# Kernel tuning notes

Measured on AMD Instinct MI355X. Metric: run time of the kernel, lower is better.

## Reference

```python
import jax, jax.numpy as jnp
import numpy as np
import math

N_NODES = 50000
N_EDGES = 1600000
C = 256
H = 8
HD = C // H


def setup_inputs() -> dict:
    key = jax.random.key(0)
    ks = jax.random.split(key, 16)
    s = 0.02
    d = {
        "feat": jax.random.normal(ks[0], (N_NODES, C), jnp.float32),
        "edge_src": jax.random.randint(ks[1], (N_EDGES,), 0, N_NODES),
        "edge_dst": jax.random.randint(ks[2], (N_EDGES,), 0, N_NODES),
        # torch nn.Linear weights are [out, in]
        "Wq": jax.random.normal(ks[3], (C, C), jnp.float32) * s,
        "bq": jnp.zeros((C,), jnp.float32),
        "Wk": jax.random.normal(ks[4], (C, C), jnp.float32) * s,
        "bk": jnp.zeros((C,), jnp.float32),
        "Wv": jax.random.normal(ks[5], (C, C), jnp.float32) * s,
        "bv": jnp.zeros((C,), jnp.float32),
        "Wp": jax.random.normal(ks[6], (C, C), jnp.float32) * s,
        "bp": jnp.zeros((C,), jnp.float32),
        "ln_g": jnp.ones((C,), jnp.float32),
        "ln_b": jnp.zeros((C,), jnp.float32),
        "W1": jax.random.normal(ks[7], (4 * C, C), jnp.float32) * s,
        "b1": jnp.zeros((4 * C,), jnp.float32),
        "W2": jax.random.normal(ks[8], (C, 4 * C), jnp.float32) * s,
        "b2": jnp.zeros((C,), jnp.float32),
    }
    return d


def _layernorm(x, g, b, eps=1e-5):
    mu = jnp.mean(x, axis=-1, keepdims=True)
    var = jnp.mean(jnp.square(x - mu), axis=-1, keepdims=True)
    return (x - mu) * jax.lax.rsqrt(var + eps) * g + b


def reference(feat, edge_src, edge_dst, Wq, bq, Wk, bk, Wv, bv, Wp, bp,
              ln_g, ln_b, W1, b1, W2, b2):
    n = feat.shape[0]
    q = (feat @ Wq.T + bq).reshape(n, H, HD)
    k = (feat @ Wk.T + bk).reshape(n, H, HD)
    v = (feat @ Wv.T + bv).reshape(n, H, HD)

    # per-edge attention logits: (q[dst] * k[src]).sum(-1) / sqrt(head_dim), clamped
    score = jnp.einsum('ehd,ehd->eh', q[edge_dst], k[edge_src])  # [E, H]
    score = jnp.clip(score / math.sqrt(HD), -10.0, 10.0)

    # destination-grouped (segment) softmax over incoming edges
    smax = jax.ops.segment_max(score, edge_dst, num_segments=n)
    smax = jnp.where(jnp.isfinite(smax), smax, 0.0)  # guard empty segments
    ex = jnp.exp(score - smax[edge_dst])
    den = jax.ops.segment_sum(ex, edge_dst, num_segments=n)
    alpha = ex / den[edge_dst]  # [E, H]

    # weighted scatter-aggregate: sum_e alpha_e * v[src_e] into dst
    wv = jax.ops.segment_sum(alpha[:, :, None] * v[edge_src], edge_dst,
                             num_segments=n).reshape(n, C)

    y = wv @ Wp.T + bp
    x = feat + y
    h = _layernorm(x, ln_g, ln_b)
    h = jax.nn.gelu(h @ W1.T + b1, approximate=False) @ W2.T + b2
    return x + h
```

## Files before the change

### kernel.cpp

```cpp
#include <hip/hip_runtime.h>
#include <hip/hip_bf16.h>

#define CDIM 256
#define NH 8
#define HDIM 32

typedef short bf8 __attribute__((ext_vector_type(8)));
typedef float f32x4 __attribute__((ext_vector_type(4)));
typedef float f32x2 __attribute__((ext_vector_type(2)));

__device__ __forceinline__ float bf2f(ushort u) {
  union { unsigned int i; float f; } x; x.i = ((unsigned int)u) << 16; return x.f;
}
__device__ __forceinline__ ushort f2bf(float f) {
  union { float f; unsigned int i; } x; x.f = f;
  unsigned int lsb = (x.i >> 16) & 1u;
  unsigned int r = x.i + 0x7fffu + lsb;
  return (ushort)(r >> 16);
}

__device__ __forceinline__ float dec_e4m3_sw(unsigned int b) {
  unsigned int s = b >> 7, e = (b >> 3) & 15, m = b & 7;
  float v = (e == 0) ? (float)m * 0.001953125f
                     : (float)(8 + m) * 0.125f * exp2f((float)((int)e - 7));
  return s ? -v : v;
}
__device__ __forceinline__ unsigned char enc_e4m3_sw(float f) {
  union { float f; unsigned int u; } x; x.f = f;
  unsigned int s = (x.u >> 31) << 7;
  float a = fabsf(f);
  if (!(a > 0.f)) return (unsigned char)s;
  if (a > 448.f) a = 448.f;
  int e = 0; float mant = frexpf(a, &e);
  int E = e + 6;
  unsigned int out;
  if (E <= 0) {
    int m = (int)rintf(a * 512.f);
    out = (m > 7) ? (s | (1u << 3)) : (s | (unsigned)m);
  } else {
    int m = (int)rintf(mant * 16.f);
    if (m == 16) { m = 8; E++; }
    if (E > 15 || (E == 15 && m - 8 > 6)) { E = 15; m = 14; }
    out = s | ((unsigned)E << 3) | (unsigned)(m - 8);
  }
  return (unsigned char)out;
}
template <bool HI>
__device__ __forceinline__ f32x2 fp8x2_f32(unsigned int w) {
#if __has_builtin(__builtin_amdgcn_cvt_pk_f32_fp8)
  return __builtin_amdgcn_cvt_pk_f32_fp8(w, HI);
#else
  unsigned int b0 = HI ? ((w >> 16) & 0xffu) : (w & 0xffu);
  unsigned int b1 = HI ? (w >> 24) : ((w >> 8) & 0xffu);
  f32x2 r; r[0] = dec_e4m3_sw(b0); r[1] = dec_e4m3_sw(b1); return r;
#endif
}
__device__ __forceinline__ unsigned char f32_fp8(float f) {
#if __has_builtin(__builtin_amdgcn_cvt_pk_fp8_f32)
  return (unsigned char)(__builtin_amdgcn_cvt_pk_fp8_f32(f, f, 0, false) & 0xff);
#else
  return enc_e4m3_sw(f);
#endif
}

__device__ __forceinline__ float fast_gelu(float t) {
  float u = 0.7978845608028654f * (t + 0.044715f * t * t * t);
  float ez = __expf(2.f * u);
  float th = 1.f - 2.f * __builtin_amdgcn_rcpf(ez + 1.f);
  return 0.5f * t * (1.f + th);
}

__device__ __forceinline__ void gload_lds16(const ushort* g, ushort* l) {
  __builtin_amdgcn_global_load_lds((const __attribute__((address_space(1))) unsigned int*)g,
                                   (__attribute__((address_space(3))) unsigned int*)l,
                                   16, 0, 0);
}

__global__ void k_cast4(const float4* __restrict__ s, ushort4* __restrict__ d, int n4) {
  int i = blockIdx.x * blockDim.x + threadIdx.x;
  if (i < n4) {
    float4 v = s[i];
    ushort4 o;
    o.x = f2bf(v.x); o.y = f2bf(v.y); o.z = f2bf(v.z); o.w = f2bf(v.w);
    d[i] = o;
  }
}

__global__ void k_hist(const int* __restrict__ dst, int E, int* __restrict__ deg) {
  int i = blockIdx.x * blockDim.x + threadIdx.x;
  if (i < E) atomicAdd(&deg[dst[i]], 1);
}

__global__ __launch_bounds__(1024) void k_scan1(const int* __restrict__ deg, int N,
                                                int* __restrict__ rowptr, int* __restrict__ bsum) {
  __shared__ int s[1024];
  int t = threadIdx.x;
  int i = blockIdx.x * 1024 + t;
  int val = (i < N) ? deg[i] : 0;
  s[t] = val;
  __syncthreads();
  for (int off = 1; off < 1024; off <<= 1) {
    int add = (t >= off) ? s[t - off] : 0;
    __syncthreads();
    s[t] += add;
    __syncthreads();
  }
  if (i < N) rowptr[i + 1] = s[t];
  if (t == 1023) bsum[blockIdx.x] = s[t];
}

__global__ void k_scan2(int* __restrict__ bsum, int nb) {
  if (threadIdx.x == 0 && blockIdx.x == 0) {
    int run = 0;
    for (int j = 0; j < nb; ++j) { int t = bsum[j]; bsum[j] = run; run += t; }
  }
}

__global__ void k_scan3(int* __restrict__ rowptr, const int* __restrict__ bsum, int N) {
  int i = blockIdx.x * blockDim.x + threadIdx.x;
  if (i < N) rowptr[i + 1] += bsum[i >> 10];
  if (i == 0) rowptr[0] = 0;
}

__global__ void k_scatter(const int* __restrict__ src, const int* __restrict__ dst, int E,
                          const int* __restrict__ rowptr, int* __restrict__ cur,
                          int* __restrict__ csr_src) {
  int i = blockIdx.x * blockDim.x + threadIdx.x;
  if (i < E) {
    int d = dst[i];
    int pos = rowptr[d] + atomicAdd(&cur[d], 1);
    csr_src[pos] = src[i];
  }
}

__device__ __forceinline__ void stageA8(const ushort* __restrict__ S, int ld,
                                        int r0, int nr, int k0,
                                        ushort* lds, int wave, int lane) {
  int g = wave * 64 + lane;
  int row = g >> 2, slot = g & 3;
  int rr = r0 + row; rr = (rr < nr) ? rr : (nr - 1);
  const ushort* src = S + (size_t)rr * ld + k0 + ((slot ^ (row & 3)) << 3);
  gload_lds16(src, &lds[(size_t)(wave * 64) * 8]);
}

__device__ __forceinline__ void stageB8(const ushort* __restrict__ S, int ld,
                                        int r0, int nr, int k0,
                                        ushort* lds, int wave, int lane) {
#pragma unroll
  for (int j = 0; j < 2; ++j) {
    int g = wave * 128 + j * 64 + lane;
    int row = g >> 2, slot = g & 3;
    int rr = r0 + row; rr = (rr < nr) ? rr : (nr - 1);
    const ushort* src = S + (size_t)rr * ld + k0 + ((slot ^ (row & 3)) << 3);
    gload_lds16(src, &lds[(size_t)(wave * 128 + j * 64) * 8]);
  }
}

__device__ __forceinline__ void gemm256_core(const ushort* __restrict__ A, int lda, int rowt, int nA,
                                             const ushort* __restrict__ B, int ldb, int colt, int nB,
                                             int K, ushort* lA, ushort* lB, f32x4* acc) {
  int tid = threadIdx.x;
  int wave = tid >> 6, lane = tid & 63;
  int m = lane & 15, quad = lane >> 4;
  int r0w = (wave & 1) * 64, c0w = (wave >> 1) * 64;
  int sw = (quad ^ (m & 3)) << 3;

  for (int k0 = 0; k0 < K; k0 += 32) {
    __syncthreads();
    stageA8(A, lda, rowt, nA, k0, lA, wave, lane);
    stageB8(B, ldb, colt, nB, k0, lB, wave, lane);
    __syncthreads();

    bf8 a[4], b[4];
#pragma unroll
    for (int ri = 0; ri < 4; ++ri)
      a[ri] = *(const bf8*)&lA[(r0w + ri * 16 + m) * 32 + sw];
#pragma unroll
    for (int cj = 0; cj < 4; ++cj)
      b[cj] = *(const bf8*)&lB[(c0w + cj * 16 + m) * 32 + sw];
#pragma unroll
    for (int ri = 0; ri < 4; ++ri)
#pragma unroll
      for (int cj = 0; cj < 4; ++cj)
        acc[ri * 4 + cj] = __builtin_amdgcn_mfma_f32_16x16x32_bf16(a[ri], b[cj], acc[ri * 4 + cj], 0, 0, 0);
  }
}

__global__ __launch_bounds__(512) void k_qkvf(const ushort* __restrict__ featb,
                                              const ushort* __restrict__ Wqkv,
                                              const float* __restrict__ bq, const float* __restrict__ bk,
                                              const float* __restrict__ bv,
                                              ushort* __restrict__ q,
                                              unsigned char* __restrict__ k8,
                                              unsigned char* __restrict__ v8, int N) {
  __shared__ ushort lA[128 * 32];
  __shared__ ushort lB[256 * 32];
  int rowt = blockIdx.x * 128;
  int which = blockIdx.y;
  const float* bias = (which == 0) ? bq : (which == 1) ? bk : bv;
  int tid = threadIdx.x;
  int wave = tid >> 6, lane = tid & 63, m = lane & 15, quad = lane >> 4;
  int r0w = (wave & 1) * 64, c0w = (wave >> 1) * 64;

  f32x4 acc[16];
#pragma unroll
  for (int j = 0; j < 16; ++j) acc[j] = (f32x4){0.f, 0.f, 0.f, 0.f};

  gemm256_core(featb, CDIM, rowt, N, Wqkv + (size_t)which * 256 * CDIM, CDIM, 0, 256,
               CDIM, lA, lB, acc);

  unsigned char* o8 = (which == 1) ? k8 : v8;
#pragma unroll
  for (int cj = 0; cj < 4; ++cj) {
    int col = c0w + cj * 16 + m;
    float bs = bias[col];
#pragma unroll
    for (int ri = 0; ri < 4; ++ri)
#pragma unroll
      for (int i = 0; i < 4; ++i) {
        int r = rowt + r0w + ri * 16 + quad * 4 + i;
        if (r < N) {
          float vv = acc[ri * 4 + cj][i] + bs;
          if (which == 0) q[(size_t)r * CDIM + col] = f2bf(vv);
          else            o8[(size_t)r * CDIM + col] = f32_fp8(vv);
        }
      }
  }
}

__global__ __launch_bounds__(512) void k_proj(const ushort* __restrict__ wv,
                                              const ushort* __restrict__ Wp,
                                              const float* __restrict__ bp,
                                              const float* __restrict__ feat,
                                              float* __restrict__ x, int N) {
  __shared__ ushort lA[128 * 32];
  __shared__ ushort lB[256 * 32];
  int rowt = blockIdx.x * 128;
  int tid = threadIdx.x;
  int wave = tid >> 6, lane = tid & 63, m = lane & 15, quad = lane >> 4;
  int r0w = (wave & 1) * 64, c0w = (wave >> 1) * 64;

  f32x4 acc[16];
#pragma unroll
  for (int j = 0; j < 16; ++j) acc[j] = (f32x4){0.f, 0.f, 0.f, 0.f};

  gemm256_core(wv, CDIM, rowt, N, Wp, CDIM, 0, 256, CDIM, lA, lB, acc);

#pragma unroll
  for (int cj = 0; cj < 4; ++cj) {
    int col = c0w + cj * 16 + m;
    float bs = bp[col];
#pragma unroll
    for (int ri = 0; ri < 4; ++ri)
#pragma unroll
      for (int i = 0; i < 4; ++i) {
        int r = rowt + r0w + ri * 16 + quad * 4 + i;
        if (r < N)
          x[(size_t)r * CDIM + col] = acc[ri * 4 + cj][i] + bs + feat[(size_t)r * CDIM + col];
      }
  }
}

__global__ __launch_bounds__(512) void k_g1(const ushort* __restrict__ h,
                                            const ushort* __restrict__ W1c,
                                            const float* __restrict__ b1c,
                                            ushort* __restrict__ hid, int N) {
  __shared__ ushort lA[128 * 32];
  __shared__ ushort lB[256 * 32];
  int rowt = blockIdx.x * 128, colt = blockIdx.y * 256;
  int tid = threadIdx.x;
  int wave = tid >> 6, lane = tid & 63, m = lane & 15, quad = lane >> 4;
  int r0w = (wave & 1) * 64, c0w = (wave >> 1) * 64;

  f32x4 acc[16];
#pragma unroll
  for (int j = 0; j < 16; ++j) acc[j] = (f32x4){0.f, 0.f, 0.f, 0.f};

  gemm256_core(h, CDIM, rowt, N, W1c, CDIM, colt, 512, CDIM, lA, lB, acc);

#pragma unroll
  for (int cj = 0; cj < 4; ++cj) {
    int col = colt + c0w + cj * 16 + m;
    float bs = b1c[col];
#pragma unroll
    for (int ri = 0; ri < 4; ++ri)
#pragma unroll
      for (int i = 0; i < 4; ++i) {
        int r = rowt + r0w + ri * 16 + quad * 4 + i;
        if (r < N) hid[(size_t)r * 512 + col] = f2bf(fast_gelu(acc[ri * 4 + cj][i] + bs));
      }
  }
}

__global__ __launch_bounds__(512) void k_g2(const ushort* __restrict__ hid,
                                            const ushort* __restrict__ W2c,
                                            const float* __restrict__ b2,
                                            float* __restrict__ out, int N, int first) {
  __shared__ ushort lA[128 * 32];
  __shared__ ushort lB[256 * 32];
  int rowt = blockIdx.x * 128;
  int tid = threadIdx.x;
  int wave = tid >> 6, lane = tid & 63, m = lane & 15, quad = lane >> 4;
  int r0w = (wave & 1) * 64, c0w = (wave >> 1) * 64;

  f32x4 acc[16];
#pragma unroll
  for (int j = 0; j < 16; ++j) acc[j] = (f32x4){0.f, 0.f, 0.f, 0.f};

  gemm256_core(hid, 512, rowt, N, W2c, 1024, 0, 256, 512, lA, lB, acc);

#pragma unroll
  for (int cj = 0; cj < 4; ++cj) {
    int col = c0w + cj * 16 + m;
    float bs = first ? b2[col] : 0.f;
#pragma unroll
    for (int ri = 0; ri < 4; ++ri)
#pragma unroll
      for (int i = 0; i < 4; ++i) {
        int r = rowt + r0w + ri * 16 + quad * 4 + i;
        if (r < N) {
          size_t idx = (size_t)r * CDIM + col;
          out[idx] = out[idx] + acc[ri * 4 + cj][i] + bs;
        }
      }
  }
}

__global__ __launch_bounds__(256) void k_edge_agg(const ushort* __restrict__ q,
                                                  const unsigned char* __restrict__ kk8,
                                                  const unsigned char* __restrict__ vv8,
                                                  const int* __restrict__ rowptr,
                                                  const int* __restrict__ csr_src,
                                                  int N,
                                                  ushort* __restrict__ wv) {
  int wave = threadIdx.x >> 6, lane = threadIdx.x & 63;
  int n = blockIdx.x * 4 + wave;
  if (n >= N) return;

  int el = lane >> 3, h = lane & 7;
  int beg = rowptr[n], end = rowptr[n + 1];
  int deg = end - beg;

  float qf[32];
  {
    const ushort* qp = q + (size_t)n * CDIM + h * HDIM;
#pragma unroll
    for (int g = 0; g < 4; ++g) {
      bf8 qv = *(const bf8*)(qp + g * 8);
#pragma unroll
      for (int j = 0; j < 8; ++j) qf[g * 8 + j] = bf2f((ushort)qv[j]);
    }
  }

  float accv[4] = {0.f, 0.f, 0.f, 0.f};
  float den_part = 0.f;

  int src_n = (el < deg) ? csr_src[beg + el] : 0;
  const unsigned char* kp0 = kk8 + (size_t)src_n * CDIM + h * HDIM;
  uint4 w0_n = *(const uint4*)kp0;
  uint4 w1_n = *(const uint4*)(kp0 + 16);

  for (int c0 = 0; c0 < deg; c0 += 8) {
    int src = src_n;
    uint4 w0 = w0_n, w1 = w1_n;
    bool vcur = (c0 + el < deg);

    src_n = (c0 + 8 + el < deg) ? csr_src[beg + c0 + 8 + el] : 0;
    const unsigned char* kpn = kk8 + (size_t)src_n * CDIM + h * HDIM;
    w0_n = *(const uint4*)kpn;
    w1_n = *(const uint4*)(kpn + 16);

    float e = 0.f;
    if (vcur) {
      unsigned int ws[8] = {w0.x, w0.y, w0.z, w0.w, w1.x, w1.y, w1.z, w1.w};
      float dot = 0.f;
#pragma unroll
      for (int j = 0; j < 8; ++j) {
        f32x2 lo = fp8x2_f32<false>(ws[j]);
        f32x2 hi = fp8x2_f32<true>(ws[j]);
        dot = fmaf(qf[j * 4 + 0], lo[0], dot);
        dot = fmaf(qf[j * 4 + 1], lo[1], dot);
        dot = fmaf(qf[j * 4 + 2], hi[0], dot);
        dot = fmaf(qf[j * 4 + 3], hi[1], dot);
      }
      float s = dot * 0.17677669529663687f;
      s = fminf(10.f, fmaxf(-10.f, s));
      e = __expf(s - 10.f);
    }
    den_part += e;

#pragma unroll
    for (int j = 0; j < 8; ++j) {
      int sj = __shfl(src, j << 3);
      float ej = __shfl(e, (j << 3) | (lane >> 3));
      unsigned int vw = *(const unsigned int*)(vv8 + (size_t)sj * CDIM + lane * 4);
      f32x2 lo = fp8x2_f32<false>(vw);
      f32x2 hi = fp8x2_f32<true>(vw);
      accv[0] = fmaf(ej, lo[0], accv[0]);
      accv[1] = fmaf(ej, lo[1], accv[1]);
      accv[2] = fmaf(ej, hi[0], accv[2]);
      accv[3] = fmaf(ej, hi[1], accv[3]);
    }
  }

  float den = den_part;
  den += __shfl_xor(den, 8);
  den += __shfl_xor(den, 16);
  den += __shfl_xor(den, 32);
  float denh = __shfl(den, lane >> 3);

  float inv = (deg > 0) ? (1.f / denh) : 0.f;
  ushort4 o;
  o.x = f2bf(accv[0] * inv);
  o.y = f2bf(accv[1] * inv);
  o.z = f2bf(accv[2] * inv);
  o.w = f2bf(accv[3] * inv);
  *(ushort4*)(wv + (size_t)n * CDIM + lane * 4) = o;
}

__global__ __launch_bounds__(256) void k_ln(const float* __restrict__ x,
                                            const float* __restrict__ g,
                                            const float* __restrict__ b,
                                            ushort* __restrict__ h,
                                            float* __restrict__ out) {
  int row = blockIdx.x * 4 + (threadIdx.x >> 6);
  int lane = threadIdx.x & 63;
  const float* xr = x + (size_t)row * CDIM;
  float4 xv = *(const float4*)(xr + lane * 4);
  *(float4*)(out + (size_t)row * CDIM + lane * 4) = xv;
  float s = xv.x + xv.y + xv.z + xv.w;
  float ss = xv.x * xv.x + xv.y * xv.y + xv.z * xv.z + xv.w * xv.w;
#pragma unroll
  for (int msk = 1; msk <= 32; msk <<= 1) {
    s += __shfl_xor(s, msk);
    ss += __shfl_xor(ss, msk);
  }
  float mu = s * (1.f / CDIM);
  float var = ss * (1.f / CDIM) - mu * mu;
  float rs = rsqrtf(var + 1e-5f);
  float xe[4] = {xv.x, xv.y, xv.z, xv.w};
#pragma unroll
  for (int t = 0; t < 4; ++t) {
    int cc = lane * 4 + t;
    h[(size_t)row * CDIM + cc] = f2bf((xe[t] - mu) * rs * g[cc] + b[cc]);
  }
}

extern "C" void kernel_launch(void* const* d_in, const int* in_sizes, int n_in,
                              void* d_out, int out_size, void* d_ws, size_t ws_size,
                              hipStream_t stream) {
  const float* feat = (const float*)d_in[0];
  const int* esrc = (const int*)d_in[1];
  const int* edst = (const int*)d_in[2];
  const float* Wq = (const float*)d_in[3];
  const float* bq = (const float*)d_in[4];
  const float* Wk = (const float*)d_in[5];
  const float* bk = (const float*)d_in[6];
  const float* Wv = (const float*)d_in[7];
  const float* bv = (const float*)d_in[8];
  const float* Wp = (const float*)d_in[9];
  const float* bp = (const float*)d_in[10];
  const float* lng = (const float*)d_in[11];
  const float* lnb = (const float*)d_in[12];
  const float* W1 = (const float*)d_in[13];
  const float* b1 = (const float*)d_in[14];
  const float* W2 = (const float*)d_in[15];
  const float* b2 = (const float*)d_in[16];

  const int N = in_sizes[0] / CDIM;
  const int E = in_sizes[1];
  const size_t NC2 = (size_t)N * CDIM * 2;
  const size_t NC1 = (size_t)N * CDIM;

  char* w = (char*)d_ws;
  ushort* q   = (ushort*)(w);
  unsigned char* k8 = (unsigned char*)(w + NC2);
  unsigned char* v8 = (unsigned char*)(w + NC2 + NC1);
  ushort* wvb = (ushort*)(w + 3 * NC2);
  ushort* featb = (ushort*)(w + 3 * NC2);
  float*  x   = (float*)(w);
  ushort* h   = (ushort*)(w + 2 * NC2);
  ushort* hid = (ushort*)(w);

  char* csr = w + 4 * NC2;
  int* rowptr  = (int*)(csr);
  int* deg     = (int*)(csr + 200064);
  int* csr_src = (int*)(csr + 400128);
  int* bsum    = (int*)(csr + 400128 + (size_t)E * 4);

  char* wb = csr + 400128 + (size_t)E * 4 + 256;
  ushort* Wqb = (ushort*)(wb);
  ushort* Wkb = (ushort*)(wb + 131072);
  ushort* Wvb = (ushort*)(wb + 262144);
  ushort* Wpb = (ushort*)(wb + 393216);
  ushort* W1b = (ushort*)(wb + 524288);
  ushort* W2b = (ushort*)(wb + 1048576);

  const int nb = (N + 1023) / 1024;
  const int RT128 = (N + 127) / 128;

  k_cast4<<<(16384 + 255) / 256, 256, 0, stream>>>((const float4*)Wq, (ushort4*)Wqb, 16384);
  k_cast4<<<(16384 + 255) / 256, 256, 0, stream>>>((const float4*)Wk, (ushort4*)Wkb, 16384);
  k_cast4<<<(16384 + 255) / 256, 256, 0, stream>>>((const float4*)Wv, (ushort4*)Wvb, 16384);
  k_cast4<<<(16384 + 255) / 256, 256, 0, stream>>>((const float4*)Wp, (ushort4*)Wpb, 16384);
  k_cast4<<<(65536 + 255) / 256, 256, 0, stream>>>((const float4*)W1, (ushort4*)W1b, 65536);
  k_cast4<<<(65536 + 255) / 256, 256, 0, stream>>>((const float4*)W2, (ushort4*)W2b, 65536);
  {
    int n4 = N * CDIM / 4;
    k_cast4<<<(n4 + 255) / 256, 256, 0, stream>>>((const float4*)feat, (ushort4*)featb, n4);
  }

  hipMemsetAsync(deg, 0, (size_t)N * 4, stream);
  k_hist<<<(E + 255) / 256, 256, 0, stream>>>(edst, E, deg);
  k_scan1<<<nb, 1024, 0, stream>>>(deg, N, rowptr, bsum);
  k_scan2<<<1, 64, 0, stream>>>(bsum, nb);
  k_scan3<<<(N + 255) / 256, 256, 0, stream>>>(rowptr, bsum, N);
  hipMemsetAsync(deg, 0, (size_t)N * 4, stream);
  k_scatter<<<(E + 255) / 256, 256, 0, stream>>>(esrc, edst, E, rowptr, deg, csr_src);

  k_qkvf<<<dim3(RT128, 3), 512, 0, stream>>>(featb, Wqb, bq, bk, bv, q, k8, v8, N);
  k_edge_agg<<<(N + 3) / 4, 256, 0, stream>>>(q, k8, v8, rowptr, csr_src, N, wvb);
  k_proj<<<RT128, 512, 0, stream>>>(wvb, Wpb, bp, feat, x, N);
  k_ln<<<N / 4, 256, 0, stream>>>(x, lng, lnb, h, (float*)d_out);

  for (int c = 0; c < 2; ++c) {
    k_g1<<<dim3(RT128, 2), 512, 0, stream>>>(h, W1b + (size_t)c * 512 * CDIM,
                                             b1 + c * 512, hid, N);
    k_g2<<<RT128, 512, 0, stream>>>(hid, W2b + (size_t)c * 512,
                                    b2, (float*)d_out, N, c == 0 ? 1 : 0);
  }
}
```

Baseline: 720.8 us.

## Double-buffer GEMM LDS tiles and prefetch V rows in edge aggregation

```diff
diff --git a/kernel.cpp b/kernel.cpp
--- a/kernel.cpp
+++ b/kernel.cpp
@@ -165,24 +165,35 @@
   int r0w = (wave & 1) * 64, c0w = (wave >> 1) * 64;
   int sw = (quad ^ (m & 3)) << 3;
 
-  for (int k0 = 0; k0 < K; k0 += 32) {
-    __syncthreads();
-    stageA8(A, lda, rowt, nA, k0, lA, wave, lane);
-    stageB8(B, ldb, colt, nB, k0, lB, wave, lane);
-    __syncthreads();
-
+  int nt = K >> 5;
+  stageA8(A, lda, rowt, nA, 0, lA, wave, lane);
+  stageB8(B, ldb, colt, nB, 0, lB, wave, lane);
+  __syncthreads();
+
+  int cur = 0;
+  for (int t = 0; t < nt; ++t) {
+    if (t + 1 < nt) {
+      stageA8(A, lda, rowt, nA, (t + 1) << 5, lA + (cur ^ 1) * (128 * 32), wave, lane);
+      stageB8(B, ldb, colt, nB, (t + 1) << 5, lB + (cur ^ 1) * (256 * 32), wave, lane);
+    }
+
+    const ushort* cA = lA + cur * (128 * 32);
+    const ushort* cB = lB + cur * (256 * 32);
     bf8 a[4], b[4];
 #pragma unroll
     for (int ri = 0; ri < 4; ++ri)
-      a[ri] = *(const bf8*)&lA[(r0w + ri * 16 + m) * 32 + sw];
+      a[ri] = *(const bf8*)&cA[(r0w + ri * 16 + m) * 32 + sw];
 #pragma unroll
     for (int cj = 0; cj < 4; ++cj)
-      b[cj] = *(const bf8*)&lB[(c0w + cj * 16 + m) * 32 + sw];
+      b[cj] = *(const bf8*)&cB[(c0w + cj * 16 + m) * 32 + sw];
 #pragma unroll
     for (int ri = 0; ri < 4; ++ri)
 #pragma unroll
       for (int cj = 0; cj < 4; ++cj)
         acc[ri * 4 + cj] = __builtin_amdgcn_mfma_f32_16x16x32_bf16(a[ri], b[cj], acc[ri * 4 + cj], 0, 0, 0);
+
+    __syncthreads();
+    cur ^= 1;
   }
 }
 
@@ -193,8 +204,8 @@
                                               ushort* __restrict__ q,
                                               unsigned char* __restrict__ k8,
                                               unsigned char* __restrict__ v8, int N) {
-  __shared__ ushort lA[128 * 32];
-  __shared__ ushort lB[256 * 32];
+  __shared__ ushort lA[2 * 128 * 32];
+  __shared__ ushort lB[2 * 256 * 32];
   int rowt = blockIdx.x * 128;
   int which = blockIdx.y;
   const float* bias = (which == 0) ? bq : (which == 1) ? bk : bv;
@@ -233,8 +244,8 @@
                                               const float* __restrict__ bp,
                                               const float* __restrict__ feat,
                                               float* __restrict__ x, int N) {
-  __shared__ ushort lA[128 * 32];
-  __shared__ ushort lB[256 * 32];
+  __shared__ ushort lA[2 * 128 * 32];
+  __shared__ ushort lB[2 * 256 * 32];
   int rowt = blockIdx.x * 128;
   int tid = threadIdx.x;
   int wave = tid >> 6, lane = tid & 63, m = lane & 15, quad = lane >> 4;
@@ -265,8 +276,8 @@
                                             const ushort* __restrict__ W1c,
                                             const float* __restrict__ b1c,
                                             ushort* __restrict__ hid, int N) {
-  __shared__ ushort lA[128 * 32];
-  __shared__ ushort lB[256 * 32];
+  __shared__ ushort lA[2 * 128 * 32];
+  __shared__ ushort lB[2 * 256 * 32];
   int rowt = blockIdx.x * 128, colt = blockIdx.y * 256;
   int tid = threadIdx.x;
   int wave = tid >> 6, lane = tid & 63, m = lane & 15, quad = lane >> 4;
@@ -296,8 +307,8 @@
                                             const ushort* __restrict__ W2c,
                                             const float* __restrict__ b2,
                                             float* __restrict__ out, int N, int first) {
-  __shared__ ushort lA[128 * 32];
-  __shared__ ushort lB[256 * 32];
+  __shared__ ushort lA[2 * 128 * 32];
+  __shared__ ushort lB[2 * 256 * 32];
   int rowt = blockIdx.x * 128;
   int tid = threadIdx.x;
   int wave = tid >> 6, lane = tid & 63, m = lane & 15, quad = lane >> 4;
@@ -359,16 +370,29 @@
   const unsigned char* kp0 = kk8 + (size_t)src_n * CDIM + h * HDIM;
   uint4 w0_n = *(const uint4*)kp0;
   uint4 w1_n = *(const uint4*)(kp0 + 16);
+  unsigned int vw_n[8];
+#pragma unroll
+  for (int j = 0; j < 8; ++j) {
+    int sj = __shfl(src_n, j << 3);
+    vw_n[j] = *(const unsigned int*)(vv8 + (size_t)sj * CDIM + lane * 4);
+  }
 
   for (int c0 = 0; c0 < deg; c0 += 8) {
-    int src = src_n;
     uint4 w0 = w0_n, w1 = w1_n;
+    unsigned int vw[8];
+#pragma unroll
+    for (int j = 0; j < 8; ++j) vw[j] = vw_n[j];
     bool vcur = (c0 + el < deg);
 
     src_n = (c0 + 8 + el < deg) ? csr_src[beg + c0 + 8 + el] : 0;
     const unsigned char* kpn = kk8 + (size_t)src_n * CDIM + h * HDIM;
     w0_n = *(const uint4*)kpn;
     w1_n = *(const uint4*)(kpn + 16);
+#pragma unroll
+    for (int j = 0; j < 8; ++j) {
+      int sj = __shfl(src_n, j << 3);
+      vw_n[j] = *(const unsigned int*)(vv8 + (size_t)sj * CDIM + lane * 4);
+    }
 
     float e = 0.f;
     if (vcur) {
@@ -391,11 +415,9 @@
 
 #pragma unroll
     for (int j = 0; j < 8; ++j) {
-      int sj = __shfl(src, j << 3);
       float ej = __shfl(e, (j << 3) | (lane >> 3));
-      unsigned int vw = *(const unsigned int*)(vv8 + (size_t)sj * CDIM + lane * 4);
-      f32x2 lo = fp8x2_f32<false>(vw);
-      f32x2 hi = fp8x2_f32<true>(vw);
+      f32x2 lo = fp8x2_f32<false>(vw[j]);
+      f32x2 hi = fp8x2_f32<true>(vw[j]);
       accv[0] = fmaf(ej, lo[0], accv[0]);
       accv[1] = fmaf(ej, lo[1], accv[1]);
       accv[2] = fmaf(ej, hi[0], accv[2]);
```

New measurement: 751.5 us. +4.3%, slower.
